# Optimization experiments

Hardware: AMD Instinct MI355X
Metric: run time of the kernel (lower is better)

The kernel has to match this reference:

```python
import jax, jax.numpy as jnp
import numpy as np

B, C, H, W = 8, 256, 64, 64
CK = C // 8  # query/key channels


def setup_inputs() -> dict:
    key = jax.random.key(0)
    ks = jax.random.split(key, 8)
    s = 1.0 / np.sqrt(C)
    return {
        "x": jax.random.normal(ks[0], (B, C, H, W), dtype=jnp.float32),
        "Wq": jax.random.normal(ks[1], (CK, C), dtype=jnp.float32) * s,
        "bq": jax.random.normal(ks[2], (CK,), dtype=jnp.float32) * 0.01,
        "Wk": jax.random.normal(ks[3], (CK, C), dtype=jnp.float32) * s,
        "bk": jax.random.normal(ks[4], (CK,), dtype=jnp.float32) * 0.01,
        "Wv": jax.random.normal(ks[5], (C, C), dtype=jnp.float32) * s,
        "bv": jax.random.normal(ks[6], (C,), dtype=jnp.float32) * 0.01,
        "gamma": jax.random.normal(ks[7], (1,), dtype=jnp.float32) * 0.1,
    }


def reference(x, Wq, bq, Wk, bk, Wv, bv, gamma):
    b, c, h, w = x.shape
    n = h * w
    xf = x.reshape(b, c, n)                       # [B,C,N]
    # 1x1 convs == channel-wise linear maps
    q = jnp.einsum('oc,bcn->bon', Wq, xf) + bq[:, None]   # [B,CK,N]
    k = jnp.einsum('oc,bcn->bon', Wk, xf) + bk[:, None]   # [B,CK,N]
    v = jnp.einsum('oc,bcn->bon', Wv, xf) + bv[:, None]   # [B,C,N]
    energy = jnp.einsum('bcm,bcn->bmn', q, k)             # [B,N,N] (query rows m)
    attn = jax.nn.softmax(energy, axis=-1)
    out = jnp.einsum('bcn,bmn->bcm', v, attn)             # value @ attn^T
    out = out.reshape(b, c, h, w)
    return gamma * out + x
```

## Files before the change

kernel.cpp:

```cpp
#include <hip/hip_runtime.h>
#include <stdint.h>

typedef unsigned short u16;
typedef unsigned int u32;
typedef __bf16 bf16_t;
typedef __bf16 bf16x4 __attribute__((ext_vector_type(4)));
typedef __bf16 bf16x8 __attribute__((ext_vector_type(8)));
typedef float f32x4 __attribute__((ext_vector_type(4)));
typedef float f32x16 __attribute__((ext_vector_type(16)));

#define LOG2E 1.4426950408889634f
#define MFMA32(a, b, c) __builtin_amdgcn_mfma_f32_32x32x16_bf16(a, b, c, 0, 0, 0)

__device__ __forceinline__ u16 f2bf(float f) {
    union { float f; unsigned int u; } v; v.f = f;
    unsigned int r = v.u + 0x7fffu + ((v.u >> 16) & 1u);
    return (u16)(r >> 16);
}

__device__ __forceinline__ bf16x8 ld8f_bf(const float* __restrict__ p) {
    float4 a = *reinterpret_cast<const float4*>(p);
    float4 b = *reinterpret_cast<const float4*>(p + 4);
    bf16x8 r;
    r[0] = (bf16_t)a.x; r[1] = (bf16_t)a.y; r[2] = (bf16_t)a.z; r[3] = (bf16_t)a.w;
    r[4] = (bf16_t)b.x; r[5] = (bf16_t)b.y; r[6] = (bf16_t)b.z; r[7] = (bf16_t)b.w;
    return r;
}

__device__ __forceinline__ u32 cvt_pk_bf16(float a, float b) {
    u32 r;
    asm("v_cvt_pk_bf16_f32 %0, %1, %2" : "=v"(r) : "v"(a), "v"(b));
    return r;
}

__device__ __forceinline__ void plane32_swap(u32& a, u32& b) {
    asm("v_permlane32_swap_b32 %0, %1" : "+v"(a), "+v"(b));
}

__device__ __forceinline__ bf16x8 pack8(const float* p) {
    u32 c0 = cvt_pk_bf16(p[0], p[1]);
    u32 c1 = cvt_pk_bf16(p[2], p[3]);
    u32 c2 = cvt_pk_bf16(p[4], p[5]);
    u32 c3 = cvt_pk_bf16(p[6], p[7]);
    plane32_swap(c0, c2);
    plane32_swap(c1, c3);
    union { u32 u[4]; bf16x8 v; } f;
    f.u[0] = c0; f.u[1] = c1; f.u[2] = c2; f.u[3] = c3;
    return f.v;
}

__device__ __forceinline__ void g2lds16(const u16* g, u16* l) {
    __builtin_amdgcn_global_load_lds(
        (const __attribute__((address_space(1))) unsigned int*)g,
        (__attribute__((address_space(3))) unsigned int*)l, 16, 0, 0);
}

__global__ __launch_bounds__(256) void k_transpose(const float* __restrict__ x,
                                                   u16* __restrict__ xT) {
    __shared__ u16 tile[64][68];
    int blk = blockIdx.x;
    int b = blk >> 8;
    int r = blk & 255;
    int c0 = (r & 3) * 64;
    int n0 = (r >> 2) * 64;
    const float* xb = x + (size_t)b * 256 * 4096;
    u16* xTb = xT + (size_t)b * 4096 * 256;
    int t = threadIdx.x;
    int lc = t >> 4;
    int l4 = (t & 15) * 4;
    #pragma unroll
    for (int p = 0; p < 4; ++p) {
        int c = lc + p * 16;
        float4 v = *reinterpret_cast<const float4*>(xb + (size_t)(c0 + c) * 4096 + n0 + l4);
        tile[c][l4 + 0] = f2bf(v.x); tile[c][l4 + 1] = f2bf(v.y);
        tile[c][l4 + 2] = f2bf(v.z); tile[c][l4 + 3] = f2bf(v.w);
    }
    __syncthreads();
    #pragma unroll
    for (int p = 0; p < 4; ++p) {
        int n = lc + p * 16;
        ushort4 v;
        v.x = tile[l4 + 0][n]; v.y = tile[l4 + 1][n];
        v.z = tile[l4 + 2][n]; v.w = tile[l4 + 3][n];
        *reinterpret_cast<ushort4*>(xTb + (size_t)(n0 + n) * 256 + c0 + l4) = v;
    }
}

__global__ __launch_bounds__(256, 2) void k_proj(
    const u16* __restrict__ xT,
    const float* __restrict__ Wq, const float* __restrict__ bq,
    const float* __restrict__ Wk, const float* __restrict__ bk,
    const float* __restrict__ Wv, const float* __restrict__ bv,
    u16* __restrict__ qt, u16* __restrict__ kt, u16* __restrict__ vt) {
    __shared__ u16 Xs[64 * 256];
    __shared__ u16 Ws[64 * 256];
    __shared__ u16 Wvs[256 * 32];
    int blk = blockIdx.x;
    int b = blk & 7;
    int n0 = (blk >> 3) * 64;
    int t = threadIdx.x;
    int w = t >> 6;
    int lane = t & 63;
    int lo = lane & 15;
    int q = lane >> 4;
    const u16* xTb = xT + (size_t)b * 4096 * 256;

    #pragma unroll
    for (int p = 0; p < 8; ++p) {
        int G = p * 256 + t;
        int n = G >> 5, g = G & 31;
        bf16x8 v = *reinterpret_cast<const bf16x8*>(
            xTb + (size_t)(n0 + n) * 256 + g * 8);
        *reinterpret_cast<bf16x8*>(&Xs[(n * 32 + (g ^ (n & 7))) * 8]) = v;
        const float* src = (n < 32) ? (Wq + (size_t)n * 256 + g * 8)
                                    : (Wk + (size_t)(n - 32) * 256 + g * 8);
        *reinterpret_cast<bf16x8*>(&Ws[(n * 32 + (g ^ (n & 7))) * 8]) = ld8f_bf(src);
    }

    f32x4 accqk[4] = {};
    f32x4 accv[16];
    #pragma unroll
    for (int i = 0; i < 16; ++i) accv[i] = f32x4{0.f, 0.f, 0.f, 0.f};

    int rowA = w * 16 + lo;
    int cw = w * 64;
    for (int c0 = 0; c0 < 256; c0 += 32) {
        __syncthreads();
        #pragma unroll
        for (int p = 0; p < 4; ++p) {
            int G = p * 256 + t;
            int co = G >> 2, g2 = G & 3;
            *reinterpret_cast<bf16x8*>(&Wvs[(co * 4 + (g2 ^ (co & 3))) * 8]) =
                ld8f_bf(Wv + (size_t)co * 256 + c0 + g2 * 8);
        }
        __syncthreads();

        int K = c0 >> 3;
        bf16x8 a = *reinterpret_cast<const bf16x8*>(
            &Xs[(rowA * 32 + ((K + q) ^ (lo & 7))) * 8]);
        #pragma unroll
        for (int ot = 0; ot < 4; ++ot) {
            bf16x8 bb = *reinterpret_cast<const bf16x8*>(
                &Ws[((ot * 16 + lo) * 32 + ((K + q) ^ (lo & 7))) * 8]);
            accqk[ot] = __builtin_amdgcn_mfma_f32_16x16x32_bf16(a, bb, accqk[ot], 0, 0, 0);
        }
        bf16x8 xbf[4];
        #pragma unroll
        for (int nt = 0; nt < 4; ++nt)
            xbf[nt] = *reinterpret_cast<const bf16x8*>(
                &Xs[((nt * 16 + lo) * 32 + ((K + q) ^ (lo & 7))) * 8]);
        #pragma unroll
        for (int ct = 0; ct < 4; ++ct) {
            int co = cw + ct * 16 + lo;
            bf16x8 av = *reinterpret_cast<const bf16x8*>(
                &Wvs[(co * 4 + (q ^ (co & 3))) * 8]);
            #pragma unroll
            for (int nt = 0; nt < 4; ++nt)
                accv[ct * 4 + nt] = __builtin_amdgcn_mfma_f32_16x16x32_bf16(
                    av, xbf[nt], accv[ct * 4 + nt], 0, 0, 0);
        }
    }
    #pragma unroll
    for (int ot = 0; ot < 4; ++ot) {
        float bias = (ot < 2) ? bq[ot * 16 + lo] : bk[(ot - 2) * 16 + lo];
        #pragma unroll
        for (int r = 0; r < 4; ++r) {
            int n = n0 + w * 16 + q * 4 + r;
            float val = accqk[ot][r] + bias;
            if (ot < 2) qt[((size_t)b * 4096 + n) * 32 + ot * 16 + lo] = f2bf(val * LOG2E);
            else        kt[((size_t)b * 4096 + n) * 32 + (ot - 2) * 16 + lo] = f2bf(val);
        }
    }
    #pragma unroll
    for (int ct = 0; ct < 4; ++ct) {
        #pragma unroll
        for (int nt = 0; nt < 4; ++nt) {
            int nt_g = (n0 >> 4) + nt;
            #pragma unroll
            for (int r = 0; r < 4; ++r) {
                int co = cw + ct * 16 + q * 4 + r;
                float val = accv[ct * 4 + nt][r] + bv[co];
                vt[(((size_t)b * 256 + nt_g) * 256 + co) * 16 + lo] = f2bf(val);
            }
        }
    }
}

__global__ __launch_bounds__(256, 2) void k_flash(
    const u16* __restrict__ qt, const u16* __restrict__ kt,
    const u16* __restrict__ vt, const float* __restrict__ x,
    const float* __restrict__ gamma, float* __restrict__ out) {
    __shared__ u16 Vs[2][8192];
    __shared__ u16 Ks[2][2048];
    int blk = blockIdx.x;
    int b = blk & 7;
    int rest = blk >> 3;
    int m0 = (rest & 31) * 128;
    int ch0 = (rest >> 5) * 128;
    int t = threadIdx.x;
    int w = t >> 6;
    int lane = t & 63;
    int la = lane & 31;
    int hi = lane >> 5;

    const u16* qtb = qt + (size_t)b * 4096 * 32;
    const u16* ktb = kt + (size_t)b * 4096 * 32;
    const u16* vtb = vt + (size_t)b * 256 * 256 * 16;

    int qw0 = m0 + w * 32;
    bf16x8 qf0 = *reinterpret_cast<const bf16x8*>(qtb + (size_t)(qw0 + la) * 32 + hi * 8);
    bf16x8 qf1 = *reinterpret_cast<const bf16x8*>(qtb + (size_t)(qw0 + la) * 32 + 16 + hi * 8);

    int g = la * 2 + hi;
    int gslot8 = (g ^ (g >> 3)) * 8;
    int sg = lane ^ (lane >> 3);

    const u16* vsrc = vtb + ((size_t)w * 256 + ch0) * 16 + sg * 8;
    const u16* ksrc = ktb + (size_t)((w >> 1) * 32 + (sg >> 1)) * 32 + (w & 1) * 16 + (sg & 1) * 8;
    u16* vdstA = &Vs[0][w * 4 * 512];
    u16* kdstA = &Ks[0][w * 512];
    u16* vdstB = &Vs[1][w * 4 * 512];
    u16* kdstB = &Ks[1][w * 512];

    #pragma unroll
    for (int i = 0; i < 4; ++i) g2lds16(vsrc + i * 512, vdstA + i * 512);
    g2lds16(ksrc, kdstA);
    vsrc += 16384;
    ksrc += 2048;

    f32x16 O0 = {}, O1 = {}, O2 = {}, O3 = {};
    const f32x16 z16 = {};
    float lsum = 0.f;
    __syncthreads();

    for (int s = 0; s < 64; ++s) {
        const u16* Vc = Vs[s & 1];
        const u16* Kc = Ks[s & 1];
        if (s < 63) {
            u16* vd = (s & 1) ? vdstA : vdstB;
            u16* kd = (s & 1) ? kdstA : kdstB;
            #pragma unroll
            for (int i = 0; i < 4; ++i) g2lds16(vsrc + i * 512, vd + i * 512);
            g2lds16(ksrc, kd);
            vsrc += 16384;
            ksrc += 2048;
        }
        bf16x8 kf00 = *reinterpret_cast<const bf16x8*>(Kc + 0 * 512 + gslot8);
        bf16x8 kf01 = *reinterpret_cast<const bf16x8*>(Kc + 1 * 512 + gslot8);
        bf16x8 kf10 = *reinterpret_cast<const bf16x8*>(Kc + 2 * 512 + gslot8);
        bf16x8 kf11 = *reinterpret_cast<const bf16x8*>(Kc + 3 * 512 + gslot8);
        f32x16 S0 = MFMA32(kf00, qf0, z16);
        S0 = MFMA32(kf01, qf1, S0);
        f32x16 S1 = MFMA32(kf10, qf0, z16);
        S1 = MFMA32(kf11, qf1, S1);
        float p0[16];
        #pragma unroll
        for (int i = 0; i < 16; ++i) {
            p0[i] = __builtin_amdgcn_exp2f(S0[i]);
            lsum += p0[i];
        }
        bf16x8 fA = pack8(p0);
        bf16x8 fB = pack8(p0 + 8);
        {
            bf16x8 v0 = *reinterpret_cast<const bf16x8*>(Vc + 0 * 512 + gslot8);
            bf16x8 v1 = *reinterpret_cast<const bf16x8*>(Vc + 1 * 512 + gslot8);
            bf16x8 v2 = *reinterpret_cast<const bf16x8*>(Vc + 2 * 512 + gslot8);
            bf16x8 v3 = *reinterpret_cast<const bf16x8*>(Vc + 3 * 512 + gslot8);
            O0 = MFMA32(v0, fA, O0);
            O1 = MFMA32(v1, fA, O1);
            O2 = MFMA32(v2, fA, O2);
            O3 = MFMA32(v3, fA, O3);
            bf16x8 v4 = *reinterpret_cast<const bf16x8*>(Vc + 4 * 512 + gslot8);
            bf16x8 v5 = *reinterpret_cast<const bf16x8*>(Vc + 5 * 512 + gslot8);
            bf16x8 v6 = *reinterpret_cast<const bf16x8*>(Vc + 6 * 512 + gslot8);
            bf16x8 v7 = *reinterpret_cast<const bf16x8*>(Vc + 7 * 512 + gslot8);
            O0 = MFMA32(v4, fB, O0);
            O1 = MFMA32(v5, fB, O1);
            O2 = MFMA32(v6, fB, O2);
            O3 = MFMA32(v7, fB, O3);
        }
        float p1[16];
        #pragma unroll
        for (int i = 0; i < 16; ++i) {
            p1[i] = __builtin_amdgcn_exp2f(S1[i]);
            lsum += p1[i];
        }
        bf16x8 fC = pack8(p1);
        bf16x8 fD = pack8(p1 + 8);
        {
            bf16x8 v0 = *reinterpret_cast<const bf16x8*>(Vc + 8 * 512 + gslot8);
            bf16x8 v1 = *reinterpret_cast<const bf16x8*>(Vc + 9 * 512 + gslot8);
            bf16x8 v2 = *reinterpret_cast<const bf16x8*>(Vc + 10 * 512 + gslot8);
            bf16x8 v3 = *reinterpret_cast<const bf16x8*>(Vc + 11 * 512 + gslot8);
            O0 = MFMA32(v0, fC, O0);
            O1 = MFMA32(v1, fC, O1);
            O2 = MFMA32(v2, fC, O2);
            O3 = MFMA32(v3, fC, O3);
            bf16x8 v4 = *reinterpret_cast<const bf16x8*>(Vc + 12 * 512 + gslot8);
            bf16x8 v5 = *reinterpret_cast<const bf16x8*>(Vc + 13 * 512 + gslot8);
            bf16x8 v6 = *reinterpret_cast<const bf16x8*>(Vc + 14 * 512 + gslot8);
            bf16x8 v7 = *reinterpret_cast<const bf16x8*>(Vc + 15 * 512 + gslot8);
            O0 = MFMA32(v4, fD, O0);
            O1 = MFMA32(v5, fD, O1);
            O2 = MFMA32(v6, fD, O2);
            O3 = MFMA32(v7, fD, O3);
        }
        __syncthreads();
    }

    lsum += __shfl_xor(lsum, 32, 64);
    float linv = 1.0f / lsum;
    float gm = gamma[0];
    const float* xb = x + (size_t)b * 256 * 4096;
    float* ob = out + (size_t)b * 256 * 4096;
    int m = m0 + w * 32 + la;
    #pragma unroll
    for (int r = 0; r < 16; ++r) {
        int crow = (r & 3) + 8 * (r >> 2) + 4 * hi;
        size_t i0 = (size_t)(ch0 + crow) * 4096 + m;
        ob[i0]             = gm * (O0[r] * linv) + xb[i0];
        ob[i0 + 32 * 4096] = gm * (O1[r] * linv) + xb[i0 + 32 * 4096];
        ob[i0 + 64 * 4096] = gm * (O2[r] * linv) + xb[i0 + 64 * 4096];
        ob[i0 + 96 * 4096] = gm * (O3[r] * linv) + xb[i0 + 96 * 4096];
    }
}

extern "C" void kernel_launch(void* const* d_in, const int* in_sizes, int n_in,
                              void* d_out, int out_size, void* d_ws, size_t ws_size,
                              hipStream_t stream) {
    const float* x     = (const float*)d_in[0];
    const float* Wq    = (const float*)d_in[1];
    const float* bq    = (const float*)d_in[2];
    const float* Wk    = (const float*)d_in[3];
    const float* bk    = (const float*)d_in[4];
    const float* Wv    = (const float*)d_in[5];
    const float* bv    = (const float*)d_in[6];
    const float* gamma = (const float*)d_in[7];
    float* out = (float*)d_out;

    char* ws = (char*)d_ws;
    u16* xT = (u16*)d_out;
    u16* qt = (u16*)ws;
    u16* kt = (u16*)(ws + 2097152);
    u16* vt = (u16*)(ws + 2 * 2097152);

    k_transpose<<<2048, 256, 0, stream>>>(x, xT);
    k_proj<<<512, 256, 0, stream>>>(xT, Wq, bq, Wk, bk, Wv, bv, qt, kt, vt);
    k_flash<<<512, 256, 0, stream>>>(qt, kt, vt, x, gamma, out);
}
```

Measured before the change: 204.4 us.

## Pre-convert weights to bf16, use async LDS loads in projection, software-pipeline flash

The transpose kernel gains extra blocks that convert Wq/Wk/Wv to bf16 once, already in the swizzled layout, and it writes xT pre-swizzled. The projection kernel can then fill shared memory with direct global-to-LDS loads instead of per-block fp32-to-bf16 conversions. The flash kernel stops staging K through LDS and reads K fragments straight from global memory into registers two steps ahead. It also software-pipelines softmax with the P·V MFMAs across iterations, with an explicit prologue and epilogue. This aims to hide load latency and overlap exp with the matrix work, at the cost of more registers and more complex code.

```diff
diff --git a/kernel.cpp b/kernel.cpp
--- a/kernel.cpp
+++ b/kernel.cpp
@@ -55,17 +55,42 @@
         (__attribute__((address_space(3))) unsigned int*)l, 16, 0, 0);
 }
 
-__global__ __launch_bounds__(256) void k_transpose(const float* __restrict__ x,
-                                                   u16* __restrict__ xT) {
+__global__ __launch_bounds__(256) void k_transpose(
+    const float* __restrict__ x,
+    const float* __restrict__ Wq, const float* __restrict__ Wk,
+    const float* __restrict__ Wv,
+    u16* __restrict__ xT, u16* __restrict__ wqkb, u16* __restrict__ wvb) {
+    int blk = blockIdx.x;
+    int t = threadIdx.x;
+    if (blk >= 2048) {
+        if (blk == 2048) {
+            for (int j = 0; j < 8; ++j) {
+                int fg = j * 256 + t;
+                int n = fg >> 5, g = fg & 31;
+                const float* src = (n < 32) ? (Wq + (size_t)n * 256 + g * 8)
+                                            : (Wk + (size_t)(n - 32) * 256 + g * 8);
+                *reinterpret_cast<bf16x8*>(wqkb + n * 256 + ((g ^ (n & 7)) << 3)) =
+                    ld8f_bf(src);
+            }
+        } else {
+            int base = (blk - 2049) * 2048;
+            for (int j = 0; j < 8; ++j) {
+                int fg = base + j * 256 + t;
+                int slice = fg >> 10, d = fg & 1023;
+                int co = d >> 2, g2 = (d & 3) ^ (co & 3);
+                *reinterpret_cast<bf16x8*>(wvb + fg * 8) =
+                    ld8f_bf(Wv + (size_t)co * 256 + slice * 32 + g2 * 8);
+            }
+        }
+        return;
+    }
     __shared__ u16 tile[64][68];
-    int blk = blockIdx.x;
     int b = blk >> 8;
     int r = blk & 255;
     int c0 = (r & 3) * 64;
     int n0 = (r >> 2) * 64;
     const float* xb = x + (size_t)b * 256 * 4096;
     u16* xTb = xT + (size_t)b * 4096 * 256;
-    int t = threadIdx.x;
     int lc = t >> 4;
     int l4 = (t & 15) * 4;
     #pragma unroll
@@ -82,15 +107,17 @@
         ushort4 v;
         v.x = tile[l4 + 0][n]; v.y = tile[l4 + 1][n];
         v.z = tile[l4 + 2][n]; v.w = tile[l4 + 3][n];
-        *reinterpret_cast<ushort4*>(xTb + (size_t)(n0 + n) * 256 + c0 + l4) = v;
+        int gslot = ((c0 + l4) >> 3) ^ ((n0 + n) & 7);
+        *reinterpret_cast<ushort4*>(
+            xTb + (size_t)(n0 + n) * 256 + (gslot << 3) + (l4 & 7)) = v;
     }
 }
 
 __global__ __launch_bounds__(256, 2) void k_proj(
-    const u16* __restrict__ xT,
-    const float* __restrict__ Wq, const float* __restrict__ bq,
-    const float* __restrict__ Wk, const float* __restrict__ bk,
-    const float* __restrict__ Wv, const float* __restrict__ bv,
+    const u16* __restrict__ xT, const u16* __restrict__ wqkb,
+    const u16* __restrict__ wvb,
+    const float* __restrict__ bq, const float* __restrict__ bk,
+    const float* __restrict__ bv,
     u16* __restrict__ qt, u16* __restrict__ kt, u16* __restrict__ vt) {
     __shared__ u16 Xs[64 * 256];
     __shared__ u16 Ws[64 * 256];
@@ -107,14 +134,8 @@
 
     #pragma unroll
     for (int p = 0; p < 8; ++p) {
-        int G = p * 256 + t;
-        int n = G >> 5, g = G & 31;
-        bf16x8 v = *reinterpret_cast<const bf16x8*>(
-            xTb + (size_t)(n0 + n) * 256 + g * 8);
-        *reinterpret_cast<bf16x8*>(&Xs[(n * 32 + (g ^ (n & 7))) * 8]) = v;
-        const float* src = (n < 32) ? (Wq + (size_t)n * 256 + g * 8)
-                                    : (Wk + (size_t)(n - 32) * 256 + g * 8);
-        *reinterpret_cast<bf16x8*>(&Ws[(n * 32 + (g ^ (n & 7))) * 8]) = ld8f_bf(src);
+        g2lds16(xTb + (size_t)n0 * 256 + (p * 256 + t) * 8, &Xs[(p * 256 + w * 64) * 8]);
+        g2lds16(wqkb + (p * 256 + t) * 8, &Ws[(p * 256 + w * 64) * 8]);
     }
 
     f32x4 accqk[4] = {};
@@ -128,10 +149,8 @@
         __syncthreads();
         #pragma unroll
         for (int p = 0; p < 4; ++p) {
-            int G = p * 256 + t;
-            int co = G >> 2, g2 = G & 3;
-            *reinterpret_cast<bf16x8*>(&Wvs[(co * 4 + (g2 ^ (co & 3))) * 8]) =
-                ld8f_bf(Wv + (size_t)co * 256 + c0 + g2 * 8);
+            g2lds16(wvb + (size_t)(c0 >> 5) * 8192 + (p * 256 + t) * 8,
+                    &Wvs[(p * 256 + w * 64) * 8]);
         }
         __syncthreads();
 
@@ -186,12 +205,77 @@
     }
 }
 
+#define FLASH_PV_HALF1(FC0, FC1, Vc_)                                          \
+    {                                                                          \
+        bf16x8 v0_ = *reinterpret_cast<const bf16x8*>(Vc_ + gslot8);           \
+        bf16x8 v1_ = *reinterpret_cast<const bf16x8*>(Vc_ + 512 + gslot8);     \
+        bf16x8 v2_ = *reinterpret_cast<const bf16x8*>(Vc_ + 1024 + gslot8);    \
+        bf16x8 v3_ = *reinterpret_cast<const bf16x8*>(Vc_ + 1536 + gslot8);    \
+        O0 = MFMA32(v0_, FC0, O0); O1 = MFMA32(v1_, FC0, O1);                  \
+        O2 = MFMA32(v2_, FC0, O2); O3 = MFMA32(v3_, FC0, O3);                  \
+        bf16x8 v4_ = *reinterpret_cast<const bf16x8*>(Vc_ + 2048 + gslot8);    \
+        bf16x8 v5_ = *reinterpret_cast<const bf16x8*>(Vc_ + 2560 + gslot8);    \
+        bf16x8 v6_ = *reinterpret_cast<const bf16x8*>(Vc_ + 3072 + gslot8);    \
+        bf16x8 v7_ = *reinterpret_cast<const bf16x8*>(Vc_ + 3584 + gslot8);    \
+        O0 = MFMA32(v4_, FC1, O0); O1 = MFMA32(v5_, FC1, O1);                  \
+        O2 = MFMA32(v6_, FC1, O2); O3 = MFMA32(v7_, FC1, O3);                  \
+    }
+
+#define FLASH_PV_HALF2(FC2, FC3, Vc_)                                          \
+    {                                                                          \
+        bf16x8 v0_ = *reinterpret_cast<const bf16x8*>(Vc_ + 4096 + gslot8);    \
+        bf16x8 v1_ = *reinterpret_cast<const bf16x8*>(Vc_ + 4608 + gslot8);    \
+        bf16x8 v2_ = *reinterpret_cast<const bf16x8*>(Vc_ + 5120 + gslot8);    \
+        bf16x8 v3_ = *reinterpret_cast<const bf16x8*>(Vc_ + 5632 + gslot8);    \
+        O0 = MFMA32(v0_, FC2, O0); O1 = MFMA32(v1_, FC2, O1);                  \
+        O2 = MFMA32(v2_, FC2, O2); O3 = MFMA32(v3_, FC2, O3);                  \
+        bf16x8 v4_ = *reinterpret_cast<const bf16x8*>(Vc_ + 6144 + gslot8);    \
+        bf16x8 v5_ = *reinterpret_cast<const bf16x8*>(Vc_ + 6656 + gslot8);    \
+        bf16x8 v6_ = *reinterpret_cast<const bf16x8*>(Vc_ + 7168 + gslot8);    \
+        bf16x8 v7_ = *reinterpret_cast<const bf16x8*>(Vc_ + 7680 + gslot8);    \
+        O0 = MFMA32(v4_, FC3, O0); O1 = MFMA32(v5_, FC3, O1);                  \
+        O2 = MFMA32(v6_, FC3, O2); O3 = MFMA32(v7_, FC3, O3);                  \
+    }
+
+#define FLASH_ITER(S_, KC0, KC1, KC2, KC3, KN0, KN1, KN2, KN3,                 \
+                   FC0, FC1, FC2, FC3, FN0, FN1, FN2, FN3, VDN)                \
+    {                                                                          \
+        const int s_ = (S_);                                                   \
+        const u16* kp_ = kbase + (size_t)(((s_ + 2) & 63) * 2048);             \
+        KN0 = *reinterpret_cast<const bf16x8*>(kp_);                           \
+        KN1 = *reinterpret_cast<const bf16x8*>(kp_ + 16);                      \
+        KN2 = *reinterpret_cast<const bf16x8*>(kp_ + 1024);                    \
+        KN3 = *reinterpret_cast<const bf16x8*>(kp_ + 1040);                    \
+        const u16* vs_ = vstage + (size_t)(s_ + 1) * 16384;                    \
+        g2lds16(vs_,        VDN);                                              \
+        g2lds16(vs_ + 512,  VDN + 512);                                        \
+        g2lds16(vs_ + 1024, VDN + 1024);                                       \
+        g2lds16(vs_ + 1536, VDN + 1536);                                       \
+        f32x16 S0_ = MFMA32(KC0, qf0, z16); S0_ = MFMA32(KC1, qf1, S0_);       \
+        f32x16 S1_ = MFMA32(KC2, qf0, z16); S1_ = MFMA32(KC3, qf1, S1_);       \
+        const u16* Vc_ = Vs[s_ & 1];                                           \
+        float p0_[16];                                                         \
+        _Pragma("unroll")                                                      \
+        for (int i_ = 0; i_ < 16; ++i_) {                                      \
+            p0_[i_] = __builtin_amdgcn_exp2f(S0_[i_]); lsum += p0_[i_];        \
+        }                                                                      \
+        FN0 = pack8(p0_); FN1 = pack8(p0_ + 8);                                \
+        FLASH_PV_HALF1(FC0, FC1, Vc_)                                          \
+        float p1_[16];                                                         \
+        _Pragma("unroll")                                                      \
+        for (int i_ = 0; i_ < 16; ++i_) {                                      \
+            p1_[i_] = __builtin_amdgcn_exp2f(S1_[i_]); lsum += p1_[i_];        \
+        }                                                                      \
+        FN2 = pack8(p1_); FN3 = pack8(p1_ + 8);                                \
+        FLASH_PV_HALF2(FC2, FC3, Vc_)                                          \
+        __syncthreads();                                                       \
+    }
+
 __global__ __launch_bounds__(256, 2) void k_flash(
     const u16* __restrict__ qt, const u16* __restrict__ kt,
     const u16* __restrict__ vt, const float* __restrict__ x,
     const float* __restrict__ gamma, float* __restrict__ out) {
     __shared__ u16 Vs[2][8192];
-    __shared__ u16 Ks[2][2048];
     int blk = blockIdx.x;
     int b = blk & 7;
     int rest = blk >> 3;
@@ -211,101 +295,60 @@
     bf16x8 qf0 = *reinterpret_cast<const bf16x8*>(qtb + (size_t)(qw0 + la) * 32 + hi * 8);
     bf16x8 qf1 = *reinterpret_cast<const bf16x8*>(qtb + (size_t)(qw0 + la) * 32 + 16 + hi * 8);
 
+    const u16* kbase = ktb + (size_t)la * 32 + hi * 8;
+
     int g = la * 2 + hi;
     int gslot8 = (g ^ (g >> 3)) * 8;
     int sg = lane ^ (lane >> 3);
-
-    const u16* vsrc = vtb + ((size_t)w * 256 + ch0) * 16 + sg * 8;
-    const u16* ksrc = ktb + (size_t)((w >> 1) * 32 + (sg >> 1)) * 32 + (w & 1) * 16 + (sg & 1) * 8;
-    u16* vdstA = &Vs[0][w * 4 * 512];
-    u16* kdstA = &Ks[0][w * 512];
-    u16* vdstB = &Vs[1][w * 4 * 512];
-    u16* kdstB = &Ks[1][w * 512];
-
-    #pragma unroll
-    for (int i = 0; i < 4; ++i) g2lds16(vsrc + i * 512, vdstA + i * 512);
-    g2lds16(ksrc, kdstA);
-    vsrc += 16384;
-    ksrc += 2048;
+    const u16* vstage = vtb + ((size_t)(w * 256) + ch0) * 16 + sg * 8;
+    u16* vd0 = &Vs[0][w * 2048];
+    u16* vd1 = &Vs[1][w * 2048];
 
     f32x16 O0 = {}, O1 = {}, O2 = {}, O3 = {};
     const f32x16 z16 = {};
     float lsum = 0.f;
+
+    bf16x8 kA0, kA1, kA2, kA3, kB0, kB1, kB2, kB3;
+    bf16x8 fA0, fA1, fA2, fA3, fB0, fB1, fB2, fB3;
+
+    kA0 = *reinterpret_cast<const bf16x8*>(kbase);
+    kA1 = *reinterpret_cast<const bf16x8*>(kbase + 16);
+    kA2 = *reinterpret_cast<const bf16x8*>(kbase + 1024);
+    kA3 = *reinterpret_cast<const bf16x8*>(kbase + 1040);
+    g2lds16(vstage,        vd0);
+    g2lds16(vstage + 512,  vd0 + 512);
+    g2lds16(vstage + 1024, vd0 + 1024);
+    g2lds16(vstage + 1536, vd0 + 1536);
+    kB0 = *reinterpret_cast<const bf16x8*>(kbase + 2048);
+    kB1 = *reinterpret_cast<const bf16x8*>(kbase + 2064);
+    kB2 = *reinterpret_cast<const bf16x8*>(kbase + 3072);
+    kB3 = *reinterpret_cast<const bf16x8*>(kbase + 3088);
+    {
+        f32x16 S0 = MFMA32(kA0, qf0, z16); S0 = MFMA32(kA1, qf1, S0);
+        f32x16 S1 = MFMA32(kA2, qf0, z16); S1 = MFMA32(kA3, qf1, S1);
+        float p0[16], p1[16];
+        #pragma unroll
+        for (int i = 0; i < 16; ++i) { p0[i] = __builtin_amdgcn_exp2f(S0[i]); lsum += p0[i]; }
+        fA0 = pack8(p0); fA1 = pack8(p0 + 8);
+        #pragma unroll
+        for (int i = 0; i < 16; ++i) { p1[i] = __builtin_amdgcn_exp2f(S1[i]); lsum += p1[i]; }
+        fA2 = pack8(p1); fA3 = pack8(p1 + 8);
+    }
     __syncthreads();
 
-    for (int s = 0; s < 64; ++s) {
-        const u16* Vc = Vs[s & 1];
-        const u16* Kc = Ks[s & 1];
-        if (s < 63) {
-            u16* vd = (s & 1) ? vdstA : vdstB;
-            u16* kd = (s & 1) ? kdstA : kdstB;
-            #pragma unroll
-            for (int i = 0; i < 4; ++i) g2lds16(vsrc + i * 512, vd + i * 512);
-            g2lds16(ksrc, kd);
-            vsrc += 16384;
-            ksrc += 2048;
-        }
-        bf16x8 kf00 = *reinterpret_cast<const bf16x8*>(Kc + 0 * 512 + gslot8);
-        bf16x8 kf01 = *reinterpret_cast<const bf16x8*>(Kc + 1 * 512 + gslot8);
-        bf16x8 kf10 = *reinterpret_cast<const bf16x8*>(Kc + 2 * 512 + gslot8);
-        bf16x8 kf11 = *reinterpret_cast<const bf16x8*>(Kc + 3 * 512 + gslot8);
-        f32x16 S0 = MFMA32(kf00, qf0, z16);
-        S0 = MFMA32(kf01, qf1, S0);
-        f32x16 S1 = MFMA32(kf10, qf0, z16);
-        S1 = MFMA32(kf11, qf1, S1);
-        float p0[16];
-        #pragma unroll
-        for (int i = 0; i < 16; ++i) {
-            p0[i] = __builtin_amdgcn_exp2f(S0[i]);
-            lsum += p0[i];
-        }
-        bf16x8 fA = pack8(p0);
-        bf16x8 fB = pack8(p0 + 8);
-        {
-            bf16x8 v0 = *reinterpret_cast<const bf16x8*>(Vc + 0 * 512 + gslot8);
-            bf16x8 v1 = *reinterpret_cast<const bf16x8*>(Vc + 1 * 512 + gslot8);
-            bf16x8 v2 = *reinterpret_cast<const bf16x8*>(Vc + 2 * 512 + gslot8);
-            bf16x8 v3 = *reinterpret_cast<const bf16x8*>(Vc + 3 * 512 + gslot8);
-            O0 = MFMA32(v0, fA, O0);
-            O1 = MFMA32(v1, fA, O1);
-            O2 = MFMA32(v2, fA, O2);
-            O3 = MFMA32(v3, fA, O3);
-            bf16x8 v4 = *reinterpret_cast<const bf16x8*>(Vc + 4 * 512 + gslot8);
-            bf16x8 v5 = *reinterpret_cast<const bf16x8*>(Vc + 5 * 512 + gslot8);
-            bf16x8 v6 = *reinterpret_cast<const bf16x8*>(Vc + 6 * 512 + gslot8);
-            bf16x8 v7 = *reinterpret_cast<const bf16x8*>(Vc + 7 * 512 + gslot8);
-            O0 = MFMA32(v4, fB, O0);
-            O1 = MFMA32(v5, fB, O1);
-            O2 = MFMA32(v6, fB, O2);
-            O3 = MFMA32(v7, fB, O3);
-        }
-        float p1[16];
-        #pragma unroll
-        for (int i = 0; i < 16; ++i) {
-            p1[i] = __builtin_amdgcn_exp2f(S1[i]);
-            lsum += p1[i];
-        }
-        bf16x8 fC = pack8(p1);
-        bf16x8 fD = pack8(p1 + 8);
-        {
-            bf16x8 v0 = *reinterpret_cast<const bf16x8*>(Vc + 8 * 512 + gslot8);
-            bf16x8 v1 = *reinterpret_cast<const bf16x8*>(Vc + 9 * 512 + gslot8);
-            bf16x8 v2 = *reinterpret_cast<const bf16x8*>(Vc + 10 * 512 + gslot8);
-            bf16x8 v3 = *reinterpret_cast<const bf16x8*>(Vc + 11 * 512 + gslot8);
-            O0 = MFMA32(v0, fC, O0);
-            O1 = MFMA32(v1, fC, O1);
-            O2 = MFMA32(v2, fC, O2);
-            O3 = MFMA32(v3, fC, O3);
-            bf16x8 v4 = *reinterpret_cast<const bf16x8*>(Vc + 12 * 512 + gslot8);
-            bf16x8 v5 = *reinterpret_cast<const bf16x8*>(Vc + 13 * 512 + gslot8);
-            bf16x8 v6 = *reinterpret_cast<const bf16x8*>(Vc + 14 * 512 + gslot8);
-            bf16x8 v7 = *reinterpret_cast<const bf16x8*>(Vc + 15 * 512 + gslot8);
-            O0 = MFMA32(v4, fD, O0);
-            O1 = MFMA32(v5, fD, O1);
-            O2 = MFMA32(v6, fD, O2);
-            O3 = MFMA32(v7, fD, O3);
-        }
-        __syncthreads();
+    for (int ss = 0; ss < 31; ++ss) {
+        int s0 = ss * 2;
+        FLASH_ITER(s0,     kB0, kB1, kB2, kB3, kA0, kA1, kA2, kA3,
+                           fA0, fA1, fA2, fA3, fB0, fB1, fB2, fB3, vd1)
+        FLASH_ITER(s0 + 1, kA0, kA1, kA2, kA3, kB0, kB1, kB2, kB3,
+                           fB0, fB1, fB2, fB3, fA0, fA1, fA2, fA3, vd0)
+    }
+    FLASH_ITER(62, kB0, kB1, kB2, kB3, kA0, kA1, kA2, kA3,
+                   fA0, fA1, fA2, fA3, fB0, fB1, fB2, fB3, vd1)
+    {
+        const u16* Vc_ = Vs[1];
+        FLASH_PV_HALF1(fB0, fB1, Vc_)
+        FLASH_PV_HALF2(fB2, fB3, Vc_)
     }
 
     lsum += __shfl_xor(lsum, 32, 64);
@@ -339,12 +382,14 @@
     float* out = (float*)d_out;
 
     char* ws = (char*)d_ws;
-    u16* xT = (u16*)d_out;
+    u16* xT   = (u16*)d_out;
+    u16* wqkb = (u16*)d_out + 8388608;
+    u16* wvb  = (u16*)d_out + 8388608 + 16384;
     u16* qt = (u16*)ws;
     u16* kt = (u16*)(ws + 2097152);
     u16* vt = (u16*)(ws + 2 * 2097152);
 
-    k_transpose<<<2048, 256, 0, stream>>>(x, xT);
-    k_proj<<<512, 256, 0, stream>>>(xT, Wq, bq, Wk, bk, Wv, bv, qt, kt, vt);
+    k_transpose<<<2053, 256, 0, stream>>>(x, Wq, Wk, Wv, xT, wqkb, wvb);
+    k_proj<<<512, 256, 0, stream>>>(xT, wqkb, wvb, bq, bk, bv, qt, kt, vt);
     k_flash<<<512, 256, 0, stream>>>(qt, kt, vt, x, gamma, out);
 }
```

New measurement: 199.9 us. 1.02x faster.

## Pre-convert weights to swizzled bf16 and stream projection tiles via direct LDS loads

Applied to the files above, without the earlier changes.

The transpose kernel gains extra blocks that convert Wq/Wk/Wv to bf16 in a pre-swizzled layout, and it writes xT already swizzled. The projection kernel now uses 512 threads over 128 positions and loads X and weights into LDS with global_load_lds. The Wv slices are double-buffered, which removes the per-step fp32-to-bf16 conversion of Wv and one of the two barriers per step. This costs more LDS per block and leaves half as many blocks, and the scratch buffers placed inside the output must not be overwritten before use.

```diff
diff --git a/kernel.cpp b/kernel.cpp
--- a/kernel.cpp
+++ b/kernel.cpp
@@ -55,17 +55,42 @@
         (__attribute__((address_space(3))) unsigned int*)l, 16, 0, 0);
 }
 
-__global__ __launch_bounds__(256) void k_transpose(const float* __restrict__ x,
-                                                   u16* __restrict__ xT) {
+__global__ __launch_bounds__(256) void k_transpose(
+    const float* __restrict__ x,
+    const float* __restrict__ Wq, const float* __restrict__ Wk,
+    const float* __restrict__ Wv,
+    u16* __restrict__ xT, u16* __restrict__ wqkb, u16* __restrict__ wvb) {
+    int blk = blockIdx.x;
+    int t = threadIdx.x;
+    if (blk >= 2048) {
+        if (blk == 2048) {
+            for (int j = 0; j < 8; ++j) {
+                int fg = j * 256 + t;
+                int n = fg >> 5, g = fg & 31;
+                const float* src = (n < 32) ? (Wq + (size_t)n * 256 + g * 8)
+                                            : (Wk + (size_t)(n - 32) * 256 + g * 8);
+                *reinterpret_cast<bf16x8*>(wqkb + n * 256 + ((g ^ (n & 7)) << 3)) =
+                    ld8f_bf(src);
+            }
+        } else {
+            int base = (blk - 2049) * 2048;
+            for (int j = 0; j < 8; ++j) {
+                int fg = base + j * 256 + t;
+                int slice = fg >> 10, d = fg & 1023;
+                int co = d >> 2, g2 = (d & 3) ^ (co & 3);
+                *reinterpret_cast<bf16x8*>(wvb + fg * 8) =
+                    ld8f_bf(Wv + (size_t)co * 256 + slice * 32 + g2 * 8);
+            }
+        }
+        return;
+    }
     __shared__ u16 tile[64][68];
-    int blk = blockIdx.x;
     int b = blk >> 8;
     int r = blk & 255;
     int c0 = (r & 3) * 64;
     int n0 = (r >> 2) * 64;
     const float* xb = x + (size_t)b * 256 * 4096;
     u16* xTb = xT + (size_t)b * 4096 * 256;
-    int t = threadIdx.x;
     int lc = t >> 4;
     int l4 = (t & 15) * 4;
     #pragma unroll
@@ -82,22 +107,24 @@
         ushort4 v;
         v.x = tile[l4 + 0][n]; v.y = tile[l4 + 1][n];
         v.z = tile[l4 + 2][n]; v.w = tile[l4 + 3][n];
-        *reinterpret_cast<ushort4*>(xTb + (size_t)(n0 + n) * 256 + c0 + l4) = v;
-    }
-}
-
-__global__ __launch_bounds__(256, 2) void k_proj(
-    const u16* __restrict__ xT,
-    const float* __restrict__ Wq, const float* __restrict__ bq,
-    const float* __restrict__ Wk, const float* __restrict__ bk,
-    const float* __restrict__ Wv, const float* __restrict__ bv,
+        int gslot = ((c0 + l4) >> 3) ^ ((n0 + n) & 7);
+        *reinterpret_cast<ushort4*>(
+            xTb + (size_t)(n0 + n) * 256 + (gslot << 3) + (l4 & 7)) = v;
+    }
+}
+
+__global__ __launch_bounds__(512, 2) void k_proj(
+    const u16* __restrict__ xT, const u16* __restrict__ wqkb,
+    const u16* __restrict__ wvb,
+    const float* __restrict__ bq, const float* __restrict__ bk,
+    const float* __restrict__ bv,
     u16* __restrict__ qt, u16* __restrict__ kt, u16* __restrict__ vt) {
-    __shared__ u16 Xs[64 * 256];
+    __shared__ u16 Xs[128 * 256];
     __shared__ u16 Ws[64 * 256];
-    __shared__ u16 Wvs[256 * 32];
+    __shared__ u16 Wvs[2][256 * 32];
     int blk = blockIdx.x;
     int b = blk & 7;
-    int n0 = (blk >> 3) * 64;
+    int n0 = (blk >> 3) * 128;
     int t = threadIdx.x;
     int w = t >> 6;
     int lane = t & 63;
@@ -106,16 +133,14 @@
     const u16* xTb = xT + (size_t)b * 4096 * 256;
 
     #pragma unroll
-    for (int p = 0; p < 8; ++p) {
-        int G = p * 256 + t;
-        int n = G >> 5, g = G & 31;
-        bf16x8 v = *reinterpret_cast<const bf16x8*>(
-            xTb + (size_t)(n0 + n) * 256 + g * 8);
-        *reinterpret_cast<bf16x8*>(&Xs[(n * 32 + (g ^ (n & 7))) * 8]) = v;
-        const float* src = (n < 32) ? (Wq + (size_t)n * 256 + g * 8)
-                                    : (Wk + (size_t)(n - 32) * 256 + g * 8);
-        *reinterpret_cast<bf16x8*>(&Ws[(n * 32 + (g ^ (n & 7))) * 8]) = ld8f_bf(src);
-    }
+    for (int p = 0; p < 8; ++p)
+        g2lds16(xTb + (size_t)n0 * 256 + (p * 512 + t) * 8, &Xs[(p * 512 + w * 64) * 8]);
+    #pragma unroll
+    for (int p = 0; p < 4; ++p)
+        g2lds16(wqkb + (p * 512 + t) * 8, &Ws[(p * 512 + w * 64) * 8]);
+    #pragma unroll
+    for (int p = 0; p < 2; ++p)
+        g2lds16(wvb + (p * 512 + t) * 8, &Wvs[0][(p * 512 + w * 64) * 8]);
 
     f32x4 accqk[4] = {};
     f32x4 accv[16];
@@ -123,18 +148,20 @@
     for (int i = 0; i < 16; ++i) accv[i] = f32x4{0.f, 0.f, 0.f, 0.f};
 
     int rowA = w * 16 + lo;
-    int cw = w * 64;
-    for (int c0 = 0; c0 < 256; c0 += 32) {
-        __syncthreads();
-        #pragma unroll
-        for (int p = 0; p < 4; ++p) {
-            int G = p * 256 + t;
-            int co = G >> 2, g2 = G & 3;
-            *reinterpret_cast<bf16x8*>(&Wvs[(co * 4 + (g2 ^ (co & 3))) * 8]) =
-                ld8f_bf(Wv + (size_t)co * 256 + c0 + g2 * 8);
-        }
-        __syncthreads();
-
+    int cw = (w & 3) * 64;
+    int nh = (w >> 2) * 64;
+    __syncthreads();
+
+    for (int s = 0; s < 8; ++s) {
+        int c0 = s * 32;
+        const u16* Wv_r = &Wvs[s & 1][0];
+        u16* Wv_w = &Wvs[(s + 1) & 1][0];
+        if (s < 7) {
+            #pragma unroll
+            for (int p = 0; p < 2; ++p)
+                g2lds16(wvb + (size_t)(s + 1) * 8192 + (p * 512 + t) * 8,
+                        Wv_w + (p * 512 + w * 64) * 8);
+        }
         int K = c0 >> 3;
         bf16x8 a = *reinterpret_cast<const bf16x8*>(
             &Xs[(rowA * 32 + ((K + q) ^ (lo & 7))) * 8]);
@@ -148,17 +175,18 @@
         #pragma unroll
         for (int nt = 0; nt < 4; ++nt)
             xbf[nt] = *reinterpret_cast<const bf16x8*>(
-                &Xs[((nt * 16 + lo) * 32 + ((K + q) ^ (lo & 7))) * 8]);
+                &Xs[((nh + nt * 16 + lo) * 32 + ((K + q) ^ (lo & 7))) * 8]);
         #pragma unroll
         for (int ct = 0; ct < 4; ++ct) {
             int co = cw + ct * 16 + lo;
             bf16x8 av = *reinterpret_cast<const bf16x8*>(
-                &Wvs[(co * 4 + (q ^ (co & 3))) * 8]);
+                Wv_r + (co * 4 + (q ^ (co & 3))) * 8);
             #pragma unroll
             for (int nt = 0; nt < 4; ++nt)
                 accv[ct * 4 + nt] = __builtin_amdgcn_mfma_f32_16x16x32_bf16(
                     av, xbf[nt], accv[ct * 4 + nt], 0, 0, 0);
         }
+        __syncthreads();
     }
     #pragma unroll
     for (int ot = 0; ot < 4; ++ot) {
@@ -175,7 +203,7 @@
     for (int ct = 0; ct < 4; ++ct) {
         #pragma unroll
         for (int nt = 0; nt < 4; ++nt) {
-            int nt_g = (n0 >> 4) + nt;
+            int nt_g = ((n0 + nh) >> 4) + nt;
             #pragma unroll
             for (int r = 0; r < 4; ++r) {
                 int co = cw + ct * 16 + q * 4 + r;
@@ -339,12 +367,14 @@
     float* out = (float*)d_out;
 
     char* ws = (char*)d_ws;
-    u16* xT = (u16*)d_out;
+    u16* xT   = (u16*)d_out;
+    u16* wqkb = (u16*)d_out + 8388608;
+    u16* wvb  = (u16*)d_out + 8388608 + 16384;
     u16* qt = (u16*)ws;
     u16* kt = (u16*)(ws + 2097152);
     u16* vt = (u16*)(ws + 2 * 2097152);
 
-    k_transpose<<<2048, 256, 0, stream>>>(x, xT);
-    k_proj<<<512, 256, 0, stream>>>(xT, Wq, bq, Wk, bk, Wv, bv, qt, kt, vt);
+    k_transpose<<<2053, 256, 0, stream>>>(x, Wq, Wk, Wv, xT, wqkb, wvb);
+    k_proj<<<256, 512, 0, stream>>>(xT, wqkb, wvb, bq, bk, bv, qt, kt, vt);
     k_flash<<<512, 256, 0, stream>>>(qt, kt, vt, x, gamma, out);
 }
```

After: 201.9 us. No clear change (-1.2%).
